# Kernel optimization log

Hardware: AMD Instinct MI355X
Metric: run time of the kernel (lower is better)

## Reference

```python
import jax, jax.numpy as jnp
import numpy as np

B, N, E = 2, 16000, 160000
NDIMS, NMEAS, NMODES = 2, 1, 128
IN_DIM, OUT_DIM, FC_DIM = 3, 1, 128
LAYERS = [64, 64, 64, 64]
INV_MIN, INV_MAX = 0.5, 2.0


def setup_inputs() -> dict:
    key = jax.random.key(0)
    ks = jax.random.split(key, 16)
    L = len(LAYERS) - 1
    C = LAYERS[0]
    scale = 1.0 / (C * C)
    u = lambda k, sh, s: jax.random.uniform(k, sh, jnp.float32, -s, s)
    inp = {}
    inp["x"] = jax.random.normal(ks[0], (B, N, IN_DIM), jnp.float32)
    inp["node_mask"] = jnp.ones((B, N, 1), jnp.int32)
    inp["nodes"] = jax.random.uniform(ks[1], (B, N, NDIMS), jnp.float32)
    inp["node_weights"] = jax.random.uniform(ks[2], (B, N, NMEAS), jnp.float32) / N
    inp["directed_edges"] = jax.random.randint(ks[3], (B, E, 2), 0, N, jnp.int32)
    inp["edge_gradient_weights"] = jax.random.normal(ks[4], (B, E, NDIMS), jnp.float32)
    inp["modes"] = jax.random.normal(ks[5], (NMODES, NDIMS, NMEAS), jnp.float32)
    # scaled_logit(1.0, 0.5, 2.0) = log(0.5/1.0)
    inp["inv_L_scale_latent"] = jnp.full((NDIMS, NMEAS), np.log((1.0 - INV_MIN) / (INV_MAX - 1.0)), jnp.float32)
    inp["fc0_W"] = u(ks[6], (C, IN_DIM), 1.0 / np.sqrt(IN_DIM))
    inp["fc0_b"] = jnp.zeros((C,), jnp.float32)
    inp["weights_c"] = u(ks[7], (L, C, C, NMODES, NMEAS), scale)
    inp["weights_s"] = u(ks[8], (L, C, C, NMODES, NMEAS), scale)
    inp["weights_0"] = u(ks[9], (L, C, C, 1, NMEAS), scale)
    inp["ws_W"] = u(ks[10], (L, C, C), 1.0 / np.sqrt(C))
    inp["ws_b"] = jnp.zeros((L, C), jnp.float32)
    inp["gws_W"] = u(ks[11], (L, C, C * NDIMS), 1.0 / np.sqrt(C * NDIMS))
    inp["gws_b"] = jnp.zeros((L, C), jnp.float32)
    inp["fc1_W"] = u(ks[12], (FC_DIM, C), 1.0 / np.sqrt(C))
    inp["fc1_b"] = jnp.zeros((FC_DIM,), jnp.float32)
    inp["fc2_W"] = u(ks[13], (OUT_DIM, FC_DIM), 1.0 / np.sqrt(FC_DIM))
    inp["fc2_b"] = jnp.zeros((OUT_DIM,), jnp.float32)
    return inp


def _forward(x, nodes, node_weights, edge_gradient_weights, modes, inv_L_scale_latent,
             fc0_W, fc0_b, weights_c, weights_s, weights_0, ws_W, ws_b, gws_W, gws_b,
             fc1_W, fc1_b, fc2_W, fc2_b, directed_edges):
    L = weights_c.shape[0]
    n = x.shape[1]
    # scaled sigmoid of latent inverse length scale
    inv_L = INV_MIN + (INV_MAX - INV_MIN) * jax.nn.sigmoid(inv_L_scale_latent)
    smodes = modes * inv_L  # [K, D, W]
    # Fourier bases over all nodes
    temp = jnp.einsum('bxd,kdw->bxkw', nodes, smodes)  # [B, N, K, W]
    bases_c, bases_s = jnp.cos(temp), jnp.sin(temp)
    bases_0 = jnp.ones(temp.shape[:2] + (1, temp.shape[-1]), temp.dtype)
    wnw = node_weights[:, :, None, :]  # [B, N, 1, W]
    wbases_c, wbases_s, wbases_0 = bases_c * wnw, bases_s * wnw, bases_0 * wnw

    tgt = directed_edges[..., 0]  # [B, E]
    src = directed_edges[..., 1]

    def grad_field(f):  # f: [B, C, N] -> [B, C*D, N]
        ft = jnp.transpose(f, (0, 2, 1))  # [B, N, C]
        f_src = jnp.take_along_axis(ft, src[..., None], axis=1)  # [B, E, C]
        f_tgt = jnp.take_along_axis(ft, tgt[..., None], axis=1)
        diff = f_src - f_tgt
        msg = jnp.einsum('bed,bec->becd', edge_gradient_weights, diff)  # [B, E, C, D]
        msg = msg.reshape(msg.shape[0], msg.shape[1], -1)  # [B, E, C*D]
        seg = jax.vmap(lambda m, t: jax.ops.segment_sum(m, t, num_segments=n))(msg, tgt)
        return jnp.transpose(seg, (0, 2, 1))  # [B, C*D, N]

    # lift: fc0 acts on channel dim
    h = jnp.einsum('oi,bni->bon', fc0_W, x) + fc0_b[None, :, None]  # [B, C, N]

    for i in range(L):
        # spectral conv with explicit bases
        x_c = jnp.einsum('bix,bxkw->bikw', h, wbases_c)
        x_s = -jnp.einsum('bix,bxkw->bikw', h, wbases_s)
        x_0 = jnp.einsum('bix,bxkw->bikw', h, wbases_0)
        f_c = jnp.einsum('bikw,iokw->bokw', x_c, weights_c[i]) - jnp.einsum('bikw,iokw->bokw', x_s, weights_s[i])
        f_s = jnp.einsum('bikw,iokw->bokw', x_s, weights_c[i]) + jnp.einsum('bikw,iokw->bokw', x_c, weights_s[i])
        f_0 = jnp.einsum('bikw,iokw->bokw', x_0, weights_0[i])
        x1 = (jnp.einsum('bokw,bxkw->box', f_0, bases_0)
              + 2 * jnp.einsum('bokw,bxkw->box', f_c, bases_c)
              - 2 * jnp.einsum('bokw,bxkw->box', f_s, bases_s))
        # pointwise linear W
        x2 = jnp.einsum('oi,bin->bon', ws_W[i], h) + ws_b[i][None, :, None]
        # differential operator D: gradient then linear
        x3 = jnp.einsum('oi,bin->bon', gws_W[i], grad_field(h)) + gws_b[i][None, :, None]
        h = x1 + x2 + x3
        if i < L - 1:
            h = jax.nn.gelu(h)

    out = jnp.transpose(h, (0, 2, 1))  # [B, N, C]
    out = jax.nn.gelu(jnp.einsum('oc,bnc->bno', fc1_W, out) + fc1_b)
    out = jnp.einsum('oc,bnc->bno', fc2_W, out) + fc2_b
    return out  # [B, N, out_dim]


def reference(x, node_mask, nodes, node_weights, directed_edges, edge_gradient_weights,
              modes, inv_L_scale_latent, fc0_W, fc0_b, weights_c, weights_s, weights_0,
              ws_W, ws_b, gws_W, gws_b, fc1_W, fc1_b, fc2_W, fc2_b):
    del node_mask  # padding mask; all-ones here, not used in the core math
    return _forward(x, nodes, node_weights, edge_gradient_weights, modes, inv_L_scale_latent,
                    fc0_W, fc0_b, weights_c, weights_s, weights_0, ws_W, ws_b, gws_W, gws_b,
                    fc1_W, fc1_b, fc2_W, fc2_b, directed_edges)
```

## Files before the change

### kernel.cpp

```cpp
#include <hip/hip_runtime.h>
#include <math.h>

#define BB 2
#define NN 16000
#define EE 160000
#define KK 128
#define CC 64
#define LL 3

typedef __attribute__((ext_vector_type(8))) short bf16x8;
typedef __attribute__((ext_vector_type(4))) float f32x4;

__device__ __forceinline__ float gelu_f(float x){
    float x3 = x * x * x;
    return 0.5f * x * (1.f + tanhf(0.7978845608028654f * (x + 0.044715f * x3)));
}
__device__ __forceinline__ ushort f2bf(float f){
    uint u = __float_as_uint(f);
    u += 0x7fff + ((u >> 16) & 1);
    return (ushort)(u >> 16);
}
__device__ __forceinline__ float bf2f(ushort h){ return __uint_as_float(((uint)h) << 16); }
__device__ __forceinline__ void fsplit(float v, ushort &hi, ushort &lo){
    hi = f2bf(v);
    lo = f2bf(v - bf2f(hi));
}
__device__ __forceinline__ uint pk2(ushort a, ushort b){ return (uint)a | ((uint)b << 16); }

__device__ __forceinline__ void write_h_outputs(
    const float* ot, const float* nws, int b, int s, int x0, int t, int doAux,
    float* __restrict__ hx, ushort* __restrict__ hxh, ushort* __restrict__ hxl,
    ushort* __restrict__ hwh, float* __restrict__ part0){
    {
        int xl = t >> 1, half = t & 1;
        size_t gb = ((size_t)b*NN + x0 + xl)*64 + half*32;
        const float* row = &ot[xl*68 + half*32];
        #pragma unroll
        for (int j = 0; j < 8; j++){
            float4 v; v.x = row[j*4]; v.y = row[j*4+1]; v.z = row[j*4+2]; v.w = row[j*4+3];
            *(float4*)&hx[gb + j*4] = v;
        }
        if (doAux){
            #pragma unroll
            for (int q = 0; q < 4; q++){
                ushort h_[8], l_[8];
                #pragma unroll
                for (int j = 0; j < 8; j++) fsplit(row[q*8 + j], h_[j], l_[j]);
                uint4 vh, vl;
                vh.x = pk2(h_[0],h_[1]); vh.y = pk2(h_[2],h_[3]); vh.z = pk2(h_[4],h_[5]); vh.w = pk2(h_[6],h_[7]);
                vl.x = pk2(l_[0],l_[1]); vl.y = pk2(l_[2],l_[3]); vl.z = pk2(l_[4],l_[5]); vl.w = pk2(l_[6],l_[7]);
                *(uint4*)&hxh[gb + q*8] = vh;
                *(uint4*)&hxl[gb + q*8] = vl;
            }
        }
    }
    if (doAux){
        int i = t & 63, g = t >> 6;
        float a = 0.f;
        #pragma unroll
        for (int rep = 0; rep < 4; rep++){
            int xs = g*32 + rep*8;
            ushort h_[8];
            #pragma unroll
            for (int j = 0; j < 8; j++){
                float v = ot[(xs + j)*68 + i] * nws[xs + j];
                a += v;
                h_[j] = f2bf(v);
            }
            uint4 vh;
            vh.x = pk2(h_[0],h_[1]); vh.y = pk2(h_[2],h_[3]); vh.z = pk2(h_[4],h_[5]); vh.w = pk2(h_[6],h_[7]);
            size_t wb = (size_t)(b*64 + i)*16000 + x0 + xs;
            *(uint4*)&hwh[wb] = vh;
        }
        part0[((size_t)(b*125 + s)*4 + g)*64 + i] = a;
    }
}

__device__ void bases_role(
    int bid, char* smem,
    const float* __restrict__ nodes, const float* __restrict__ modes,
    const float* __restrict__ latent,
    ushort* __restrict__ cbh, ushort* __restrict__ sbh,
    ushort* __restrict__ wTh){
    int b = bid / 250, x0 = (bid % 250) * 64;
    int t = threadIdx.x;
    float* sm0 = (float*)smem;
    float* sm1 = sm0 + 128;
    uint* tc = (uint*)(sm1 + 128);
    uint* ts = tc + 64*65;
    if (t < 128){
        float i0 = 0.5f + 1.5f / (1.f + expf(-latent[0]));
        float i1 = 0.5f + 1.5f / (1.f + expf(-latent[1]));
        sm0[t] = modes[t*2+0] * i0;
        sm1[t] = modes[t*2+1] * i1;
    }
    __syncthreads();
    int xloc = t & 63;
    float n0 = nodes[((size_t)b*NN + x0 + xloc)*2 + 0];
    float n1 = nodes[((size_t)b*NN + x0 + xloc)*2 + 1];
    for (int kh = 0; kh < 2; kh++){
        int kq = t >> 6;
        #pragma unroll
        for (int j = 0; j < 16; j++){
            int kl = kq*16 + j;
            int k = kh*64 + kl;
            float tmp = n0*sm0[k] + n1*sm1[k];
            float sv, cv; sincosf(tmp, &sv, &cv);
            tc[xloc*65 + kl] = (uint)f2bf(cv);
            ts[xloc*65 + kl] = (uint)f2bf(sv);
        }
        __syncthreads();
        {
            int q = t >> 6;
            size_t base = ((size_t)b*NN + x0 + xloc)*128 + kh*64 + q*16;
            #pragma unroll
            for (int g2 = 0; g2 < 2; g2++){
                uint u0 = tc[xloc*65 + q*16 + g2*8 + 0], u1 = tc[xloc*65 + q*16 + g2*8 + 1];
                uint u2 = tc[xloc*65 + q*16 + g2*8 + 2], u3 = tc[xloc*65 + q*16 + g2*8 + 3];
                uint u4 = tc[xloc*65 + q*16 + g2*8 + 4], u5 = tc[xloc*65 + q*16 + g2*8 + 5];
                uint u6 = tc[xloc*65 + q*16 + g2*8 + 6], u7 = tc[xloc*65 + q*16 + g2*8 + 7];
                uint4 vh;
                vh.x = pk2((ushort)u0,(ushort)u1); vh.y = pk2((ushort)u2,(ushort)u3);
                vh.z = pk2((ushort)u4,(ushort)u5); vh.w = pk2((ushort)u6,(ushort)u7);
                *(uint4*)&cbh[base + g2*8] = vh;
                u0 = ts[xloc*65 + q*16 + g2*8 + 0]; u1 = ts[xloc*65 + q*16 + g2*8 + 1];
                u2 = ts[xloc*65 + q*16 + g2*8 + 2]; u3 = ts[xloc*65 + q*16 + g2*8 + 3];
                u4 = ts[xloc*65 + q*16 + g2*8 + 4]; u5 = ts[xloc*65 + q*16 + g2*8 + 5];
                u6 = ts[xloc*65 + q*16 + g2*8 + 6]; u7 = ts[xloc*65 + q*16 + g2*8 + 7];
                vh.x = pk2((ushort)u0,(ushort)u1); vh.y = pk2((ushort)u2,(ushort)u3);
                vh.z = pk2((ushort)u4,(ushort)u5); vh.w = pk2((ushort)u6,(ushort)u7);
                *(uint4*)&sbh[base + g2*8] = vh;
            }
        }
        {
            int k = t & 63, g = t >> 6;
            int kgc = kh*64 + k;
            int kgs = 128 + kh*64 + k;
            ushort hc[16], hs[16];
            #pragma unroll
            for (int j = 0; j < 16; j++){
                int xx = g*16 + j;
                hc[j] = (ushort)tc[xx*65 + k];
                hs[j] = (ushort)ts[xx*65 + k];
            }
            size_t wbc = ((size_t)b*256 + kgc)*16000 + x0 + g*16;
            size_t wbs = ((size_t)b*256 + kgs)*16000 + x0 + g*16;
            uint4 v;
            v.x = pk2(hc[0],hc[1]); v.y = pk2(hc[2],hc[3]); v.z = pk2(hc[4],hc[5]); v.w = pk2(hc[6],hc[7]);
            *(uint4*)&wTh[wbc] = v;
            v.x = pk2(hc[8],hc[9]); v.y = pk2(hc[10],hc[11]); v.z = pk2(hc[12],hc[13]); v.w = pk2(hc[14],hc[15]);
            *(uint4*)&wTh[wbc + 8] = v;
            v.x = pk2(hs[0],hs[1]); v.y = pk2(hs[2],hs[3]); v.z = pk2(hs[4],hs[5]); v.w = pk2(hs[6],hs[7]);
            *(uint4*)&wTh[wbs] = v;
            v.x = pk2(hs[8],hs[9]); v.y = pk2(hs[10],hs[11]); v.z = pk2(hs[12],hs[13]); v.w = pk2(hs[14],hs[15]);
            *(uint4*)&wTh[wbs + 8] = v;
        }
        __syncthreads();
    }
}

__device__ void fc0_role(
    int bid, char* smem,
    const float* __restrict__ x, const float* __restrict__ W,
    const float* __restrict__ bb, const float* __restrict__ nw,
    float* __restrict__ hx, ushort* __restrict__ hxh, ushort* __restrict__ hxl,
    ushort* __restrict__ hwh, float* __restrict__ part0){
    int b = bid / 125, s = bid % 125;
    int x0 = s * 128;
    int t = threadIdx.x;
    float* ot  = (float*)smem;
    float* nws = ot + 128*68;
    float* Wf  = nws + 128;
    float* bf_ = Wf + 192;
    if (t < 192) Wf[t] = W[t];
    if (t < 64) bf_[t] = bb[t];
    if (t < 128) nws[t] = nw[b*NN + x0 + t];
    __syncthreads();
    {
        int xl = t >> 1, half = t & 1;
        float v0 = x[((size_t)b*NN + x0 + xl)*3 + 0];
        float v1 = x[((size_t)b*NN + x0 + xl)*3 + 1];
        float v2 = x[((size_t)b*NN + x0 + xl)*3 + 2];
        #pragma unroll
        for (int j = 0; j < 32; j++){
            int o = half*32 + j;
            ot[xl*68 + o] = Wf[o*3]*v0 + Wf[o*3+1]*v1 + Wf[o*3+2]*v2 + bf_[o];
        }
    }
    __syncthreads();
    write_h_outputs(ot, nws, b, s, x0, t, 1, hx, hxh, hxl, hwh, part0);
}

__global__ __launch_bounds__(256) void k_start(
    const float* __restrict__ nodes, const float* __restrict__ modes,
    const float* __restrict__ latent, const float* __restrict__ nw,
    const float* __restrict__ x, const float* __restrict__ fc0W,
    const float* __restrict__ fc0b,
    ushort* __restrict__ cbh, ushort* __restrict__ sbh, ushort* __restrict__ wTh,
    float* __restrict__ hx, ushort* __restrict__ hxh, ushort* __restrict__ hxl,
    ushort* __restrict__ hwh, float* __restrict__ part0,
    int* __restrict__ cnt){
    __shared__ __align__(16) char smem[36864];
    int bid = blockIdx.x;
    if (bid < BB*250){
        bases_role(bid, smem, nodes, modes, latent, cbh, sbh, wTh);
    } else if (bid < BB*250 + BB*125){
        fc0_role(bid - BB*250, smem, x, fc0W, fc0b, nw, hx, hxh, hxl, hwh, part0);
    } else {
        int idx = (bid - (BB*250 + BB*125))*256 + threadIdx.x;
        cnt[idx] = 0;
    }
}

__global__ __launch_bounds__(256) void csr_hist(
    const int* __restrict__ edges, int* __restrict__ cnt){
    int idx = blockIdx.x * 256 + threadIdx.x;
    if (idx >= BB*EE) return;
    int b = idx / EE;
    int tgt = edges[(size_t)idx*2];
    atomicAdd(&cnt[b*NN + tgt], 1);
}

__global__ __launch_bounds__(1024) void csr_scan(
    const int* __restrict__ cnt, int* __restrict__ rowptr, int* __restrict__ cursor){
    int b = blockIdx.x;
    int t = threadIdx.x;
    __shared__ int lds[1024];
    int base = t * 16;
    int v[16];
    int run = 0;
    #pragma unroll
    for (int j = 0; j < 16; j++){
        int n = base + j;
        int c = (n < NN) ? cnt[b*NN + n] : 0;
        v[j] = run;
        run += c;
    }
    lds[t] = run;
    __syncthreads();
    for (int off = 1; off < 1024; off <<= 1){
        int xv = (t >= off) ? lds[t-off] : 0;
        __syncthreads();
        lds[t] += xv;
        __syncthreads();
    }
    int toff = lds[t] - run;
    #pragma unroll
    for (int j = 0; j < 16; j++){
        int n = base + j;
        if (n < NN){
            int p = toff + v[j];
            rowptr[b*(NN+1) + n] = p;
            cursor[b*NN + n] = p;
        }
    }
    if (t == 1023) rowptr[b*(NN+1) + NN] = lds[1023];
}

__global__ __launch_bounds__(256) void csr_fill(
    const int* __restrict__ edges, const float* __restrict__ egw,
    int* __restrict__ cursor, int* __restrict__ insrc, float2* __restrict__ inw){
    int idx = blockIdx.x * 256 + threadIdx.x;
    if (idx >= BB*EE) return;
    int b = idx / EE;
    int tgt = edges[(size_t)idx*2];
    int src = edges[(size_t)idx*2 + 1];
    int pos = atomicAdd(&cursor[b*NN + tgt], 1);
    insrc[(size_t)b*EE + pos] = src;
    const float2 wv = *(const float2*)&egw[(size_t)idx*2];
    inw[(size_t)b*EE + pos] = wv;
}

__global__ __launch_bounds__(256) void k1_fwd(
    const ushort* __restrict__ hwH,
    const ushort* __restrict__ wTH,
    uint* __restrict__ partu){
    int bid = blockIdx.x;
    int b = bid / 250, s = bid % 250;
    int x0 = s * 64;
    int t = threadIdx.x, l = t & 63, w = t >> 6;
    __shared__ __align__(16) ushort Bh[128*64];
    f32x4 acc[16] = {};
    bf16x8 Ah[2];
    int i = w*16 + (l & 15);
    #pragma unroll
    for (int ks = 0; ks < 2; ks++){
        size_t ab = (size_t)(b*64 + i)*16000 + x0 + ks*32 + ((l >> 4) * 8);
        Ah[ks] = *reinterpret_cast<const bf16x8*>(&hwH[ab]);
    }
    for (int p = 0; p < 2; p++){
        if (p) __syncthreads();
        #pragma unroll
        for (int it = 0; it < 4; it++){
            int u = it*256 + t;
            int kloc = u >> 3, q = u & 7;
            size_t g = ((size_t)(b*256 + p*128 + kloc))*16000 + x0 + q*8;
            uint4 vh = *(const uint4*)&wTH[g];
            int ldsb = kloc*128 + ((q*16) ^ ((kloc & 7) << 4));
            *(uint4*)&Bh[ldsb >> 1] = vh;
        }
        __syncthreads();
        #pragma unroll
        for (int kt = 0; kt < 8; kt++){
            int kcol = kt*16 + (l & 15);
            int ai = p*8 + kt;
            #pragma unroll
            for (int ks = 0; ks < 2; ks++){
                int boff = kcol*128 + (((ks*64) + ((l >> 4) * 16)) ^ ((kcol & 7) << 4));
                bf16x8 bh = *reinterpret_cast<const bf16x8*>(&Bh[boff >> 1]);
                acc[ai] = __builtin_amdgcn_mfma_f32_16x16x32_bf16(Ah[ks], bh, acc[ai], 0, 0, 0);
            }
        }
    }
    size_t pb = (size_t)(b*250 + s) * 64 * 128;
    #pragma unroll
    for (int nt = 0; nt < 8; nt++){
        #pragma unroll
        for (int r = 0; r < 4; r++){
            int irow = w*16 + (l >> 4)*4 + r;
            partu[pb + (size_t)irow*128 + nt*16 + (l & 15)] =
                pk2(f2bf(acc[nt][r]), f2bf(acc[nt+8][r]));
        }
    }
}

__global__ __launch_bounds__(512) void k1_reduce(
    const uint* __restrict__ partu, float* __restrict__ Sc, float* __restrict__ Ss){
    int b = blockIdx.x >> 6, i = blockIdx.x & 63;
    int t = threadIdx.x;
    int j = t & 127, sh = t >> 7;
    const uint* pb = partu + ((size_t)(b*250)*64 + i)*128 + j;
    float c0=0,c1=0,s0a=0,s1a=0;
    int s2 = sh;
    for (; s2 + 4 < 250; s2 += 8){
        uint v0 = pb[(size_t)s2*8192];
        uint v1 = pb[(size_t)(s2+4)*8192];
        c0 += bf2f((ushort)v0); s0a += bf2f((ushort)(v0 >> 16));
        c1 += bf2f((ushort)v1); s1a += bf2f((ushort)(v1 >> 16));
    }
    for (; s2 < 250; s2 += 4){
        uint v0 = pb[(size_t)s2*8192];
        c0 += bf2f((ushort)v0); s0a += bf2f((ushort)(v0 >> 16));
    }
    float cs = c0 + c1, ss = s0a + s1a;
    __shared__ float rC[4][128], rS[4][128];
    rC[sh][j] = cs; rS[sh][j] = ss;
    __syncthreads();
    if (sh == 0){
        cs = rC[0][j] + rC[1][j] + rC[2][j] + rC[3][j];
        ss = rS[0][j] + rS[1][j] + rS[2][j] + rS[3][j];
        Sc[(size_t)(b*64 + i)*128 + j] = cs;
        Ss[(size_t)(b*64 + i)*128 + j] = ss;
    }
}

__global__ __launch_bounds__(256) void k2_mix(
    const float* __restrict__ Sc, const float* __restrict__ Ss,
    const float* __restrict__ part0,
    const float* __restrict__ wc, const float* __restrict__ wsp,
    const float* __restrict__ w0,
    const float* __restrict__ wsb, const float* __restrict__ gwsb,
    const float* __restrict__ wsW, const float* __restrict__ gwsW,
    ushort* __restrict__ WbH, ushort* __restrict__ WbL,
    float* __restrict__ bias, int l){
    int b = blockIdx.x >> 6, o = blockIdx.x & 63;
    int t = threadIdx.x;
    __shared__ float fc2s[2][128], fs2s[2][128];
    __shared__ float redp[4][64];
    __shared__ float red[64];
    {
        int i = t & 63, grp = t >> 6;
        float a = 0.f;
        for (int s2 = grp; s2 < 500; s2 += 4)
            a += part0[(size_t)(b*500 + s2)*64 + i];
        redp[grp][i] = a;
    }
    int k = t & 127, hf = t >> 7;
    float fc = 0.f, fs = 0.f;
    for (int i = hf*32; i < hf*32 + 32; i++){
        float sc = Sc[(size_t)(b*CC + i)*KK + k];
        float ss = Ss[(size_t)(b*CC + i)*KK + k];
        size_t wi = (((size_t)l*CC + i)*CC + o)*KK + k;
        float a = wc[wi], bb2 = wsp[wi];
        fc += sc*a + ss*bb2;
        fs += sc*bb2 - ss*a;
    }
    fc2s[hf][k] = fc; fs2s[hf][k] = fs;
    __syncthreads();
    if (t < 64)
        red[t] = (redp[0][t]+redp[1][t]+redp[2][t]+redp[3][t]) * w0[((size_t)l*CC + t)*CC + o];
    size_t wb = (size_t)(b*CC + o) * 448;
    if (t < 128){
        float FC = fc2s[0][t] + fc2s[1][t];
        float FS = fs2s[0][t] + fs2s[1][t];
        ushort h_, l_;
        fsplit(2.f*FC, h_, l_);
        WbH[wb + t] = h_; WbL[wb + t] = l_;
        fsplit(-2.f*FS, h_, l_);
        WbH[wb + 128 + t] = h_; WbL[wb + 128 + t] = l_;
    }
    if (t >= 128 && t < 192){
        int q = t - 128;
        float v = wsW[((size_t)l*CC + o)*CC + q];
        ushort h_, l_; fsplit(v, h_, l_);
        WbH[wb + 256 + q] = h_; WbL[wb + 256 + q] = l_;
    }
    if (t >= 128){
        int q = t - 128;
        float v = gwsW[((size_t)l*CC + o)*128 + q];
        ushort h_, l_; fsplit(v, h_, l_);
        WbH[wb + 320 + q] = h_; WbL[wb + 320 + q] = l_;
    }
    __syncthreads();
    if (t == 0){
        float f0 = 0.f;
        for (int i = 0; i < 64; i++) f0 += red[i];
        bias[b*CC + o] = f0 + wsb[l*CC + o] + gwsb[l*CC + o];
    }
}

__global__ __launch_bounds__(256) void k_grad(
    const float* __restrict__ h, const int* __restrict__ rowptr,
    const int* __restrict__ insrc, const float2* __restrict__ inw,
    ushort* __restrict__ segh, ushort* __restrict__ segl){
    int bid = blockIdx.x;
    int b = bid / 2000, n0 = (bid % 2000) * 8;
    int w = threadIdx.x >> 6, c = threadIdx.x & 63;
    const float*  hb  = h + (size_t)b*NN*CC;
    const int*    isb = insrc + (size_t)b*EE;
    const float2* iwb = inw + (size_t)b*EE;
    #pragma unroll
    for (int g = 0; g < 2; g++){
        int n = n0 + w*2 + g;
        float hn = hb[(size_t)n*CC + c];
        int p0 = rowptr[b*(NN+1) + n];
        int p1 = rowptr[b*(NN+1) + n + 1];
        float a0 = 0.f, a1 = 0.f;
        int p = p0;
        for (; p + 4 <= p1; p += 4){
            int s0 = isb[p], s1 = isb[p+1], s2 = isb[p+2], s3 = isb[p+3];
            float2 w0 = iwb[p], w1 = iwb[p+1], w2 = iwb[p+2], w3 = iwb[p+3];
            float d0 = hb[(size_t)s0*CC + c] - hn;
            float d1 = hb[(size_t)s1*CC + c] - hn;
            float d2 = hb[(size_t)s2*CC + c] - hn;
            float d3 = hb[(size_t)s3*CC + c] - hn;
            a0 += w0.x*d0 + w1.x*d1 + w2.x*d2 + w3.x*d3;
            a1 += w0.y*d0 + w1.y*d1 + w2.y*d2 + w3.y*d3;
        }
        for (; p < p1; p++){
            int sx = isb[p]; float2 ww = iwb[p];
            float d = hb[(size_t)sx*CC + c] - hn;
            a0 += ww.x*d; a1 += ww.y*d;
        }
        ushort h0_, l0_, h1_, l1_;
        fsplit(a0, h0_, l0_);
        fsplit(a1, h1_, l1_);
        size_t sb2 = ((size_t)b*NN + n)*128 + 2*c;
        *(uint*)&segh[sb2] = pk2(h0_, h1_);
        *(uint*)&segl[sb2] = pk2(l0_, l1_);
    }
}

__global__ __launch_bounds__(256) void k3_gemm(
    const ushort* __restrict__ WbH, const ushort* __restrict__ WbL,
    const float* __restrict__ bias,
    const ushort* __restrict__ cbh, const ushort* __restrict__ sbh,
    const ushort* __restrict__ hxh, const ushort* __restrict__ hxl,
    const ushort* __restrict__ sgh, const ushort* __restrict__ sgl,
    const float* __restrict__ nw,
    float* __restrict__ hxO, ushort* __restrict__ hxhO, ushort* __restrict__ hxlO,
    ushort* __restrict__ hwhO, float* __restrict__ part0,
    int doAux){
    int bid = blockIdx.x;
    int b = bid / 125, s = bid % 125, x0 = s * 128;
    int t = threadIdx.x, l = t & 63, w = t >> 6;
    __shared__ __align__(16) char smem[34816];
    ushort* Vh = (ushort*)smem;
    ushort* Vl = Vh + 8192;
    __shared__ float nws[128];
    if (t < 128) nws[t] = nw[b*NN + x0 + t];
    f32x4 acc[8] = {};
    int o = w*16 + (l & 15);
    for (int cc = 0; cc < 7; cc++){
        const ushort *srcH, *srcL; int rl, co, lo;
        switch (cc){
            case 0:  srcH = cbh; srcL = cbh; rl = 128; co = 0;  lo = 0; break;
            case 1:  srcH = cbh; srcL = cbh; rl = 128; co = 64; lo = 0; break;
            case 2:  srcH = sbh; srcL = sbh; rl = 128; co = 0;  lo = 0; break;
            case 3:  srcH = sbh; srcL = sbh; rl = 128; co = 64; lo = 0; break;
            case 4:  srcH = hxh; srcL = hxl; rl = 64;  co = 0;  lo = 1; break;
            case 5:  srcH = sgh; srcL = sgl; rl = 128; co = 0;  lo = 1; break;
            default: srcH = sgh; srcL = sgl; rl = 128; co = 64; lo = 1; break;
        }
        __syncthreads();
        #pragma unroll
        for (int it = 0; it < 4; it++){
            int u = it*256 + t;
            int xl2 = u >> 3, q = u & 7;
            size_t g = (size_t)(b*NN + x0 + xl2)*rl + co + q*8;
            uint4 vh = *(const uint4*)&srcH[g];
            int ldsb = xl2*128 + ((q*16) ^ ((xl2 & 7) << 4));
            *(uint4*)&Vh[ldsb >> 1] = vh;
            if (lo){
                uint4 vl2 = *(const uint4*)&srcL[g];
                *(uint4*)&Vl[ldsb >> 1] = vl2;
            }
        }
        __syncthreads();
        bf16x8 Ah[2], Al[2];
        #pragma unroll
        for (int ks = 0; ks < 2; ks++){
            size_t ab = (size_t)(b*64 + o)*448 + cc*64 + ks*32 + ((l >> 4) * 8);
            Ah[ks] = *reinterpret_cast<const bf16x8*>(&WbH[ab]);
            Al[ks] = *reinterpret_cast<const bf16x8*>(&WbL[ab]);
        }
        #pragma unroll
        for (int nt = 0; nt < 8; nt++){
            int xc = nt*16 + (l & 15);
            #pragma unroll
            for (int ks = 0; ks < 2; ks++){
                int boff = xc*128 + (((ks*64) + ((l >> 4) * 16)) ^ ((xc & 7) << 4));
                bf16x8 bh = *reinterpret_cast<const bf16x8*>(&Vh[boff >> 1]);
                acc[nt] = __builtin_amdgcn_mfma_f32_16x16x32_bf16(Ah[ks], bh, acc[nt], 0, 0, 0);
                if (lo){
                    bf16x8 bl = *reinterpret_cast<const bf16x8*>(&Vl[boff >> 1]);
                    acc[nt] = __builtin_amdgcn_mfma_f32_16x16x32_bf16(Ah[ks], bl, acc[nt], 0, 0, 0);
                    acc[nt] = __builtin_amdgcn_mfma_f32_16x16x32_bf16(Al[ks], bh, acc[nt], 0, 0, 0);
                }
            }
        }
    }
    __syncthreads();
    float* ot = (float*)smem;
    float bv[4];
    #pragma unroll
    for (int r = 0; r < 4; r++) bv[r] = bias[b*64 + w*16 + (l >> 4)*4 + r];
    #pragma unroll
    for (int nt = 0; nt < 8; nt++){
        int xc = nt*16 + (l & 15);
        #pragma unroll
        for (int r = 0; r < 4; r++){
            float v = acc[nt][r] + bv[r];
            if (doAux) v = gelu_f(v);
            ot[xc*68 + (w*16 + (l >> 4)*4 + r)] = v;
        }
    }
    __syncthreads();
    write_h_outputs(ot, nws, b, s, x0, t, doAux, hxO, hxhO, hxlO, hwhO, part0);
}

__global__ __launch_bounds__(256) void k_head(
    const float* __restrict__ h, const float* __restrict__ W1,
    const float* __restrict__ b1, const float* __restrict__ W2,
    const float* __restrict__ b2, float* __restrict__ out){
    int bid = blockIdx.x;
    int b = bid / 250, n0 = (bid % 250) * 64;
    int t = threadIdx.x, w = t >> 6, f = t & 63;
    __shared__ float Wl[128][65];
    #pragma unroll
    for (int r = 0; r < 8; r++){
        int u = r*256 + t;
        int ff = u >> 4, cq = u & 15;
        float4 v = *(const float4*)&W1[ff*64 + cq*4];
        Wl[ff][cq*4+0] = v.x; Wl[ff][cq*4+1] = v.y;
        Wl[ff][cq*4+2] = v.z; Wl[ff][cq*4+3] = v.w;
    }
    __syncthreads();
    float w2a = W2[f], w2b = W2[64+f];
    float b1a = b1[f], b1b = b1[64+f];
    float b2v = b2[0];
    for (int g = 0; g < 16; g++){
        int n = n0 + w*16 + g;
        float hv = h[((size_t)b*NN + n)*CC + f];
        float a1 = b1a, a2 = b1b;
        #pragma unroll
        for (int c2 = 0; c2 < 64; c2++){
            float xv = __shfl(hv, c2, 64);
            a1 += Wl[f][c2] * xv;
            a2 += Wl[64+f][c2] * xv;
        }
        float p = gelu_f(a1)*w2a + gelu_f(a2)*w2b;
        for (int off = 32; off; off >>= 1) p += __shfl_down(p, off, 64);
        if (f == 0) out[(size_t)b*NN + n] = p + b2v;
    }
}

extern "C" void kernel_launch(void* const* d_in, const int* in_sizes, int n_in,
                              void* d_out, int out_size, void* d_ws, size_t ws_size,
                              hipStream_t stream){
    const float* x_in  = (const float*)d_in[0];
    const float* nodes = (const float*)d_in[2];
    const float* nw    = (const float*)d_in[3];
    const int*   edges = (const int*)d_in[4];
    const float* egw   = (const float*)d_in[5];
    const float* modes = (const float*)d_in[6];
    const float* latent= (const float*)d_in[7];
    const float* fc0W  = (const float*)d_in[8];
    const float* fc0b  = (const float*)d_in[9];
    const float* wc    = (const float*)d_in[10];
    const float* wsp   = (const float*)d_in[11];
    const float* w0    = (const float*)d_in[12];
    const float* wsW   = (const float*)d_in[13];
    const float* wsb   = (const float*)d_in[14];
    const float* gwsW  = (const float*)d_in[15];
    const float* gwsb  = (const float*)d_in[16];
    const float* fc1W  = (const float*)d_in[17];
    const float* fc1b  = (const float*)d_in[18];
    const float* fc2W  = (const float*)d_in[19];
    const float* fc2b  = (const float*)d_in[20];
    float* out = (float*)d_out;

    char* wsbase = (char*)d_ws;
    size_t off = 0;
    auto alloc = [&](size_t bytes) -> void* {
        void* p = wsbase + off;
        off += (bytes + 255) & ~(size_t)255;
        return p;
    };
    ushort* cbh = (ushort*)alloc((size_t)BB*NN*128*2);
    ushort* sbh = (ushort*)alloc((size_t)BB*NN*128*2);
    ushort* wTh = (ushort*)alloc((size_t)BB*256*NN*2);
    float*  hx[2];  ushort* hxh[2]; ushort* hxl[2]; ushort* hwh[2];
    for (int i = 0; i < 2; i++){
        hx[i]  = (float*) alloc((size_t)BB*NN*64*4);
        hxh[i] = (ushort*)alloc((size_t)BB*NN*64*2);
        hxl[i] = (ushort*)alloc((size_t)BB*NN*64*2);
        hwh[i] = (ushort*)alloc((size_t)BB*64*NN*2);
    }
    ushort* segh = (ushort*)alloc((size_t)BB*NN*128*2);
    ushort* segl = (ushort*)alloc((size_t)BB*NN*128*2);
    uint*   partu= (uint*)  alloc((size_t)BB*250*64*128*4);
    float*  part0= (float*) alloc((size_t)BB*125*4*64*4);
    float*  Sc   = (float*) alloc((size_t)BB*64*128*4);
    float*  Ss   = (float*) alloc((size_t)BB*64*128*4);
    ushort* WbH  = (ushort*)alloc((size_t)BB*64*448*2);
    ushort* WbL  = (ushort*)alloc((size_t)BB*64*448*2);
    float*  bias = (float*) alloc((size_t)BB*64*4);
    int*   cnt   = (int*)   alloc((size_t)BB*NN*4);
    int*   rowptr= (int*)   alloc((size_t)BB*(NN+4)*4);
    int*   cursor= (int*)   alloc((size_t)BB*NN*4);
    int*   insrc = (int*)   alloc((size_t)BB*EE*4);
    float2* inw  = (float2*)alloc((size_t)BB*EE*8);

    k_start<<<BB*250 + BB*125 + 125, 256, 0, stream>>>(
        nodes, modes, latent, nw, x_in, fc0W, fc0b,
        cbh, sbh, wTh,
        hx[0], hxh[0], hxl[0], hwh[0], part0, cnt);

    csr_hist<<<(BB*EE+255)/256, 256, 0, stream>>>(edges, cnt);
    csr_scan<<<BB, 1024, 0, stream>>>(cnt, rowptr, cursor);
    csr_fill<<<(BB*EE+255)/256, 256, 0, stream>>>(edges, egw, cursor, insrc, inw);

    int cur = 0;
    for (int l = 0; l < LL; l++){
        int nxt = cur ^ 1;
        int doAux = (l < LL-1) ? 1 : 0;
        k1_fwd<<<BB*250, 256, 0, stream>>>(hwh[cur], wTh, partu);
        k1_reduce<<<BB*64, 512, 0, stream>>>(partu, Sc, Ss);
        k2_mix<<<BB*64, 256, 0, stream>>>(Sc, Ss, part0, wc, wsp, w0, wsb, gwsb,
                                          wsW, gwsW, WbH, WbL, bias, l);
        k_grad<<<BB*2000, 256, 0, stream>>>(hx[cur], rowptr, insrc, inw, segh, segl);
        k3_gemm<<<BB*125, 256, 0, stream>>>(WbH, WbL, bias,
                                            cbh, sbh,
                                            hxh[cur], hxl[cur], segh, segl, nw,
                                            hx[nxt], hxh[nxt], hxl[nxt],
                                            hwh[nxt], part0, doAux);
        cur = nxt;
    }
    k_head<<<BB*250, 256, 0, stream>>>(hx[cur], fc1W, fc1b, fc2W, fc2b, out);
    (void)in_sizes; (void)n_in; (void)out_size; (void)ws_size;
}
```

Before: 527.3 us.

## Halve k3_gemm node tile and double-buffer LDS stages with register prefetch

The k3_gemm tile shrinks from 128 to 64 nodes per block, which doubles the grid to 500 blocks so more of the GPU is occupied. The seven K-chunks are now software-pipelined: the next chunk's global loads go into registers while MFMAs run on the current LDS buffer, then they are written to the other buffer. The fc0 role and the part0 partial-sum layout are changed to the same 64-node granularity, and k2_mix now reduces 1000 partials instead of 500. The cost is more partials to reduce, more blocks, and extra registers held for the prefetch.

```diff
diff --git a/kernel.cpp b/kernel.cpp
--- a/kernel.cpp
+++ b/kernel.cpp
@@ -27,52 +27,51 @@
 }
 __device__ __forceinline__ uint pk2(ushort a, ushort b){ return (uint)a | ((uint)b << 16); }
 
-__device__ __forceinline__ void write_h_outputs(
+__device__ __forceinline__ void write_h_outputs64(
     const float* ot, const float* nws, int b, int s, int x0, int t, int doAux,
     float* __restrict__ hx, ushort* __restrict__ hxh, ushort* __restrict__ hxl,
     ushort* __restrict__ hwh, float* __restrict__ part0){
     {
-        int xl = t >> 1, half = t & 1;
-        size_t gb = ((size_t)b*NN + x0 + xl)*64 + half*32;
-        const float* row = &ot[xl*68 + half*32];
-        #pragma unroll
-        for (int j = 0; j < 8; j++){
+        int xl = t >> 2, q = t & 3;
+        size_t gb = ((size_t)b*NN + x0 + xl)*64 + q*16;
+        const float* row = &ot[xl*68 + q*16];
+        #pragma unroll
+        for (int j = 0; j < 4; j++){
             float4 v; v.x = row[j*4]; v.y = row[j*4+1]; v.z = row[j*4+2]; v.w = row[j*4+3];
             *(float4*)&hx[gb + j*4] = v;
         }
         if (doAux){
             #pragma unroll
-            for (int q = 0; q < 4; q++){
+            for (int j2 = 0; j2 < 2; j2++){
                 ushort h_[8], l_[8];
                 #pragma unroll
-                for (int j = 0; j < 8; j++) fsplit(row[q*8 + j], h_[j], l_[j]);
+                for (int j = 0; j < 8; j++) fsplit(row[j2*8 + j], h_[j], l_[j]);
                 uint4 vh, vl;
                 vh.x = pk2(h_[0],h_[1]); vh.y = pk2(h_[2],h_[3]); vh.z = pk2(h_[4],h_[5]); vh.w = pk2(h_[6],h_[7]);
                 vl.x = pk2(l_[0],l_[1]); vl.y = pk2(l_[2],l_[3]); vl.z = pk2(l_[4],l_[5]); vl.w = pk2(l_[6],l_[7]);
-                *(uint4*)&hxh[gb + q*8] = vh;
-                *(uint4*)&hxl[gb + q*8] = vl;
+                *(uint4*)&hxh[gb + j2*8] = vh;
+                *(uint4*)&hxl[gb + j2*8] = vl;
             }
         }
     }
     if (doAux){
         int i = t & 63, g = t >> 6;
+        int xs = g*16;
         float a = 0.f;
-        #pragma unroll
-        for (int rep = 0; rep < 4; rep++){
-            int xs = g*32 + rep*8;
-            ushort h_[8];
-            #pragma unroll
-            for (int j = 0; j < 8; j++){
-                float v = ot[(xs + j)*68 + i] * nws[xs + j];
-                a += v;
-                h_[j] = f2bf(v);
-            }
-            uint4 vh;
-            vh.x = pk2(h_[0],h_[1]); vh.y = pk2(h_[2],h_[3]); vh.z = pk2(h_[4],h_[5]); vh.w = pk2(h_[6],h_[7]);
-            size_t wb = (size_t)(b*64 + i)*16000 + x0 + xs;
-            *(uint4*)&hwh[wb] = vh;
-        }
-        part0[((size_t)(b*125 + s)*4 + g)*64 + i] = a;
+        ushort h_[16];
+        #pragma unroll
+        for (int j = 0; j < 16; j++){
+            float v = ot[(xs + j)*68 + i] * nws[xs + j];
+            a += v;
+            h_[j] = f2bf(v);
+        }
+        size_t wb = (size_t)(b*64 + i)*16000 + x0 + xs;
+        uint4 vh;
+        vh.x = pk2(h_[0],h_[1]); vh.y = pk2(h_[2],h_[3]); vh.z = pk2(h_[4],h_[5]); vh.w = pk2(h_[6],h_[7]);
+        *(uint4*)&hwh[wb] = vh;
+        vh.x = pk2(h_[8],h_[9]); vh.y = pk2(h_[10],h_[11]); vh.z = pk2(h_[12],h_[13]); vh.w = pk2(h_[14],h_[15]);
+        *(uint4*)&hwh[wb + 8] = vh;
+        part0[((size_t)(b*250 + s)*4 + g)*64 + i] = a;
     }
 }
 
@@ -165,30 +164,29 @@
     const float* __restrict__ bb, const float* __restrict__ nw,
     float* __restrict__ hx, ushort* __restrict__ hxh, ushort* __restrict__ hxl,
     ushort* __restrict__ hwh, float* __restrict__ part0){
-    int b = bid / 125, s = bid % 125;
-    int x0 = s * 128;
+    int b = bid / 250, s = bid % 250;
+    int x0 = s * 64;
     int t = threadIdx.x;
     float* ot  = (float*)smem;
-    float* nws = ot + 128*68;
-    float* Wf  = nws + 128;
+    float* nws = ot + 64*68;
+    float* Wf  = nws + 64;
     float* bf_ = Wf + 192;
     if (t < 192) Wf[t] = W[t];
-    if (t < 64) bf_[t] = bb[t];
-    if (t < 128) nws[t] = nw[b*NN + x0 + t];
+    if (t < 64){ bf_[t] = bb[t]; nws[t] = nw[b*NN + x0 + t]; }
     __syncthreads();
     {
-        int xl = t >> 1, half = t & 1;
+        int xl = t >> 2, q = t & 3;
         float v0 = x[((size_t)b*NN + x0 + xl)*3 + 0];
         float v1 = x[((size_t)b*NN + x0 + xl)*3 + 1];
         float v2 = x[((size_t)b*NN + x0 + xl)*3 + 2];
         #pragma unroll
-        for (int j = 0; j < 32; j++){
-            int o = half*32 + j;
+        for (int j = 0; j < 16; j++){
+            int o = q*16 + j;
             ot[xl*68 + o] = Wf[o*3]*v0 + Wf[o*3+1]*v1 + Wf[o*3+2]*v2 + bf_[o];
         }
     }
     __syncthreads();
-    write_h_outputs(ot, nws, b, s, x0, t, 1, hx, hxh, hxl, hwh, part0);
+    write_h_outputs64(ot, nws, b, s, x0, t, 1, hx, hxh, hxl, hwh, part0);
 }
 
 __global__ __launch_bounds__(256) void k_start(
@@ -204,10 +202,10 @@
     int bid = blockIdx.x;
     if (bid < BB*250){
         bases_role(bid, smem, nodes, modes, latent, cbh, sbh, wTh);
-    } else if (bid < BB*250 + BB*125){
+    } else if (bid < BB*500){
         fc0_role(bid - BB*250, smem, x, fc0W, fc0b, nw, hx, hxh, hxl, hwh, part0);
     } else {
-        int idx = (bid - (BB*250 + BB*125))*256 + threadIdx.x;
+        int idx = (bid - BB*500)*256 + threadIdx.x;
         cnt[idx] = 0;
     }
 }
@@ -371,8 +369,8 @@
     {
         int i = t & 63, grp = t >> 6;
         float a = 0.f;
-        for (int s2 = grp; s2 < 500; s2 += 4)
-            a += part0[(size_t)(b*500 + s2)*64 + i];
+        for (int s2 = grp; s2 < 1000; s2 += 4)
+            a += part0[(size_t)(b*1000 + s2)*64 + i];
         redp[grp][i] = a;
     }
     int k = t & 127, hf = t >> 7;
@@ -472,40 +470,58 @@
     ushort* __restrict__ hwhO, float* __restrict__ part0,
     int doAux){
     int bid = blockIdx.x;
-    int b = bid / 125, s = bid % 125, x0 = s * 128;
+    int b = bid / 250, s = bid % 250, x0 = s * 64;
     int t = threadIdx.x, l = t & 63, w = t >> 6;
-    __shared__ __align__(16) char smem[34816];
-    ushort* Vh = (ushort*)smem;
-    ushort* Vl = Vh + 8192;
-    __shared__ float nws[128];
-    if (t < 128) nws[t] = nw[b*NN + x0 + t];
-    f32x4 acc[8] = {};
+    __shared__ __align__(16) char smem[32768];
+    __shared__ float nws[64];
+    if (t < 64) nws[t] = nw[b*NN + x0 + t];
+    f32x4 acc[4] = {};
     int o = w*16 + (l & 15);
-    for (int cc = 0; cc < 7; cc++){
-        const ushort *srcH, *srcL; int rl, co, lo;
+
+    auto desc = [&](int cc, const ushort*& sH, const ushort*& sL, int& rl, int& co, int& lof){
         switch (cc){
-            case 0:  srcH = cbh; srcL = cbh; rl = 128; co = 0;  lo = 0; break;
-            case 1:  srcH = cbh; srcL = cbh; rl = 128; co = 64; lo = 0; break;
-            case 2:  srcH = sbh; srcL = sbh; rl = 128; co = 0;  lo = 0; break;
-            case 3:  srcH = sbh; srcL = sbh; rl = 128; co = 64; lo = 0; break;
-            case 4:  srcH = hxh; srcL = hxl; rl = 64;  co = 0;  lo = 1; break;
-            case 5:  srcH = sgh; srcL = sgl; rl = 128; co = 0;  lo = 1; break;
-            default: srcH = sgh; srcL = sgl; rl = 128; co = 64; lo = 1; break;
-        }
-        __syncthreads();
-        #pragma unroll
-        for (int it = 0; it < 4; it++){
+            case 0:  sH = cbh; sL = cbh; rl = 128; co = 0;  lof = 0; break;
+            case 1:  sH = cbh; sL = cbh; rl = 128; co = 64; lof = 0; break;
+            case 2:  sH = sbh; sL = sbh; rl = 128; co = 0;  lof = 0; break;
+            case 3:  sH = sbh; sL = sbh; rl = 128; co = 64; lof = 0; break;
+            case 4:  sH = hxh; sL = hxl; rl = 64;  co = 0;  lof = 1; break;
+            case 5:  sH = sgh; sL = sgl; rl = 128; co = 0;  lof = 1; break;
+            default: sH = sgh; sL = sgl; rl = 128; co = 64; lof = 1; break;
+        }
+    };
+
+    uint4 rh[2], rlo[2];
+    auto loadStage = [&](int cc, int& lof){
+        const ushort *sH, *sL; int rl, co;
+        desc(cc, sH, sL, rl, co, lof);
+        #pragma unroll
+        for (int it = 0; it < 2; it++){
             int u = it*256 + t;
             int xl2 = u >> 3, q = u & 7;
             size_t g = (size_t)(b*NN + x0 + xl2)*rl + co + q*8;
-            uint4 vh = *(const uint4*)&srcH[g];
+            rh[it] = *(const uint4*)&sH[g];
+            if (lof) rlo[it] = *(const uint4*)&sL[g];
+        }
+    };
+    auto writeBuf = [&](int cur, int lof){
+        char* base = smem + cur*16384;
+        #pragma unroll
+        for (int it = 0; it < 2; it++){
+            int u = it*256 + t;
+            int xl2 = u >> 3, q = u & 7;
             int ldsb = xl2*128 + ((q*16) ^ ((xl2 & 7) << 4));
-            *(uint4*)&Vh[ldsb >> 1] = vh;
-            if (lo){
-                uint4 vl2 = *(const uint4*)&srcL[g];
-                *(uint4*)&Vl[ldsb >> 1] = vl2;
-            }
-        }
+            *(uint4*)(base + ldsb) = rh[it];
+            if (lof) *(uint4*)(base + 8192 + ldsb) = rlo[it];
+        }
+    };
+
+    int lo_c;
+    loadStage(0, lo_c);
+    writeBuf(0, lo_c);
+    int cur = 0;
+    for (int cc = 0; cc < 7; cc++){
+        int lo_n = 0;
+        if (cc < 6) loadStage(cc + 1, lo_n);
         __syncthreads();
         bf16x8 Ah[2], Al[2];
         #pragma unroll
@@ -514,21 +530,27 @@
             Ah[ks] = *reinterpret_cast<const bf16x8*>(&WbH[ab]);
             Al[ks] = *reinterpret_cast<const bf16x8*>(&WbL[ab]);
         }
-        #pragma unroll
-        for (int nt = 0; nt < 8; nt++){
+        char* base = smem + cur*16384;
+        #pragma unroll
+        for (int nt = 0; nt < 4; nt++){
             int xc = nt*16 + (l & 15);
             #pragma unroll
             for (int ks = 0; ks < 2; ks++){
                 int boff = xc*128 + (((ks*64) + ((l >> 4) * 16)) ^ ((xc & 7) << 4));
-                bf16x8 bh = *reinterpret_cast<const bf16x8*>(&Vh[boff >> 1]);
+                bf16x8 bh = *reinterpret_cast<const bf16x8*>(base + boff);
                 acc[nt] = __builtin_amdgcn_mfma_f32_16x16x32_bf16(Ah[ks], bh, acc[nt], 0, 0, 0);
-                if (lo){
-                    bf16x8 bl = *reinterpret_cast<const bf16x8*>(&Vl[boff >> 1]);
+                if (lo_c){
+                    bf16x8 bl = *reinterpret_cast<const bf16x8*>(base + 8192 + boff);
                     acc[nt] = __builtin_amdgcn_mfma_f32_16x16x32_bf16(Ah[ks], bl, acc[nt], 0, 0, 0);
                     acc[nt] = __builtin_amdgcn_mfma_f32_16x16x32_bf16(Al[ks], bh, acc[nt], 0, 0, 0);
                 }
             }
         }
+        if (cc < 6){
+            writeBuf(cur ^ 1, lo_n);
+            cur ^= 1;
+        }
+        lo_c = lo_n;
     }
     __syncthreads();
     float* ot = (float*)smem;
@@ -536,7 +558,7 @@
     #pragma unroll
     for (int r = 0; r < 4; r++) bv[r] = bias[b*64 + w*16 + (l >> 4)*4 + r];
     #pragma unroll
-    for (int nt = 0; nt < 8; nt++){
+    for (int nt = 0; nt < 4; nt++){
         int xc = nt*16 + (l & 15);
         #pragma unroll
         for (int r = 0; r < 4; r++){
@@ -546,7 +568,7 @@
         }
     }
     __syncthreads();
-    write_h_outputs(ot, nws, b, s, x0, t, doAux, hxO, hxhO, hxlO, hwhO, part0);
+    write_h_outputs64(ot, nws, b, s, x0, t, doAux, hxO, hxhO, hxlO, hwhO, part0);
 }
 
 __global__ __launch_bounds__(256) void k_head(
@@ -630,7 +652,7 @@
     ushort* segh = (ushort*)alloc((size_t)BB*NN*128*2);
     ushort* segl = (ushort*)alloc((size_t)BB*NN*128*2);
     uint*   partu= (uint*)  alloc((size_t)BB*250*64*128*4);
-    float*  part0= (float*) alloc((size_t)BB*125*4*64*4);
+    float*  part0= (float*) alloc((size_t)BB*1000*64*4);
     float*  Sc   = (float*) alloc((size_t)BB*64*128*4);
     float*  Ss   = (float*) alloc((size_t)BB*64*128*4);
     ushort* WbH  = (ushort*)alloc((size_t)BB*64*448*2);
@@ -642,7 +664,7 @@
     int*   insrc = (int*)   alloc((size_t)BB*EE*4);
     float2* inw  = (float2*)alloc((size_t)BB*EE*8);
 
-    k_start<<<BB*250 + BB*125 + 125, 256, 0, stream>>>(
+    k_start<<<BB*500 + 125, 256, 0, stream>>>(
         nodes, modes, latent, nw, x_in, fc0W, fc0b,
         cbh, sbh, wTh,
         hx[0], hxh[0], hxl[0], hwh[0], part0, cnt);
@@ -660,7 +682,7 @@
         k2_mix<<<BB*64, 256, 0, stream>>>(Sc, Ss, part0, wc, wsp, w0, wsb, gwsb,
                                           wsW, gwsW, WbH, WbL, bias, l);
         k_grad<<<BB*2000, 256, 0, stream>>>(hx[cur], rowptr, insrc, inw, segh, segl);
-        k3_gemm<<<BB*125, 256, 0, stream>>>(WbH, WbL, bias,
+        k3_gemm<<<BB*250, 256, 0, stream>>>(WbH, WbL, bias,
                                             cbh, sbh,
                                             hxh[cur], hxl[cur], segh, segl, nw,
                                             hx[nxt], hxh[nxt], hxl[nxt],
```

Result: slower. 592.1 us (+12.3%).
